# Kernel tuning notes

Hardware: AMD Instinct MI355X
Metric: run time of the kernel (lower is better)

## Reference

```python
import jax, jax.numpy as jnp
import numpy as np

L = 8        # number of node layers in the DAG
D = 64       # width of every node layer
B = 262144   # batch
N_CONN = L * (L - 1) // 2  # 28 all-to-all forward connections


def setup_inputs() -> dict:
    key = jax.random.key(0)
    kx, kw, kb = jax.random.split(key, 3)
    x = jax.random.normal(kx, (B, D), dtype=jnp.float32)
    # connection weights, torch Linear convention: y = x @ W.T + b, W is [out, in]
    Ws = jax.random.normal(kw, (N_CONN, D, D), dtype=jnp.float32) * (1.0 / np.sqrt(D))
    bs = jax.random.normal(kb, (N_CONN, D), dtype=jnp.float32) * 0.1
    return {"x": x, "Ws": Ws, "bs": bs}


def reference(x, Ws, bs):
    # outputs[0] = input; outputs[1..L-1] start at zero and accumulate messages.
    outs = [x] + [jnp.zeros((x.shape[0], D), dtype=x.dtype) for _ in range(L - 1)]
    # Same iteration order as the torch double loop: source i ascending,
    # target offset i2 ascending; connection c maps layer i -> layer i+i2+1.
    c = 0
    for i in range(L):
        for i2 in range(L - 1 - i):
            j = i + i2 + 1
            outs[j] = outs[j] + jax.nn.relu(outs[i] @ Ws[c].T + bs[c])
            c += 1
    return outs[L - 1]
```

## Files before the change

### kernel.cpp

```cpp
#include <hip/hip_runtime.h>


#define DD 64
#define NCONN 28
#define THREADS 256
#define ROWS_PER_WAVE 32
#define ROWS_PER_BLOCK 128
#define MAT_ELEMS 4096

typedef __bf16 bf16x8 __attribute__((ext_vector_type(8)));
typedef float f32x4 __attribute__((ext_vector_type(4)));
typedef unsigned short u16x8 __attribute__((ext_vector_type(8)));

__device__ constexpr int OFFS[7] = {0, 7, 13, 18, 22, 25, 27};
__device__ constexpr int CONN[28] = {0, 1,7, 2,8,13, 3,9,14,18, 4,10,15,19,22,
                                     5,11,16,20,23,25, 6,12,17,21,24,26,27};

__device__ __forceinline__ unsigned short f2bfu(float f) {
    return __builtin_bit_cast(unsigned short, (__bf16)f);
}

__device__ __forceinline__ f32x4 vmax4(f32x4 a, f32x4 b) {
#if __has_builtin(__builtin_elementwise_max)
    return __builtin_elementwise_max(a, b);
#else
    f32x4 r;
    r[0] = fmaxf(a[0], b[0]); r[1] = fmaxf(a[1], b[1]);
    r[2] = fmaxf(a[2], b[2]); r[3] = fmaxf(a[3], b[3]);
    return r;
#endif
}

__device__ __forceinline__ void gll16(const unsigned short* g, unsigned short* l) {
    __builtin_amdgcn_global_load_lds(
        (const __attribute__((address_space(1))) unsigned int*)g,
        (__attribute__((address_space(3))) unsigned int*)l, 16, 0, 0);
}

__global__ void wconv_kernel(const float* __restrict__ w,
                             unsigned short* __restrict__ o) {
    int i = blockIdx.x * blockDim.x + threadIdx.x;
    if (i >= NCONN * 512) return;
    int conn = i >> 9;
    int within = i & 511;
    int r  = within >> 3;
    int k0 = (within & 7) << 3;
    const float* src = w + conn * MAT_ELEMS + r * DD + k0;
    float4 v0 = *reinterpret_cast<const float4*>(src);
    float4 v1 = *reinterpret_cast<const float4*>(src + 4);
    u16x8 d;
    d[0] = f2bfu(v0.x); d[1] = f2bfu(v0.y); d[2] = f2bfu(v0.z); d[3] = f2bfu(v0.w);
    d[4] = f2bfu(v1.x); d[5] = f2bfu(v1.y); d[6] = f2bfu(v1.z); d[7] = f2bfu(v1.w);
    *reinterpret_cast<u16x8*>(o + conn * MAT_ELEMS + r * DD + (k0 ^ ((r & 7) << 3))) = d;
}

template <bool GLL>
__global__ __launch_bounds__(THREADS, 2)
void dag_kernel(const float* __restrict__ x,
                const float* __restrict__ Wf,
                const unsigned short* __restrict__ Wimg,
                const float* __restrict__ bs,
                float* __restrict__ out) {
    __shared__ __align__(16) unsigned short ring[4 * MAT_ELEMS];
    __shared__ __align__(16) unsigned short sB[4 * 1024];
    __shared__ __align__(16) float sBias[NCONN * DD];

    const int tid  = threadIdx.x;
    const int lane = tid & 63;
    const int wv   = tid >> 6;
    const int l15  = lane & 15;
    const int kg   = lane >> 4;

    const long rowbase = (long)blockIdx.x * ROWS_PER_BLOCK + wv * ROWS_PER_WAVE;

    for (int idx = tid; idx < NCONN * DD / 4; idx += THREADS)
        reinterpret_cast<float4*>(sBias)[idx] = reinterpret_cast<const float4*>(bs)[idx];

    bf16x8 afrag[7][2][2];
#pragma unroll
    for (int rt = 0; rt < 2; ++rt) {
        const float* xr = x + (rowbase + rt * 16 + l15) * DD;
#pragma unroll
        for (int s = 0; s < 2; ++s) {
            float4 v0 = *reinterpret_cast<const float4*>(xr + s * 32 + kg * 8);
            float4 v1 = *reinterpret_cast<const float4*>(xr + s * 32 + kg * 8 + 4);
            bf16x8 f;
            f[0] = (__bf16)v0.x; f[1] = (__bf16)v0.y; f[2] = (__bf16)v0.z; f[3] = (__bf16)v0.w;
            f[4] = (__bf16)v1.x; f[5] = (__bf16)v1.y; f[6] = (__bf16)v1.z; f[7] = (__bf16)v1.w;
            afrag[0][rt][s] = f;
        }
    }

    auto stage_gll = [&](int p) {
        const unsigned short* src = Wimg + CONN[p] * MAT_ELEMS + wv * 512 + lane * 8;
        unsigned short* dst = ring + (p & 3) * MAT_ELEMS + wv * 512;
#pragma unroll
        for (int h = 0; h < 2; ++h)
            gll16(src + h * 2048, dst + h * 2048);
    };
    auto stage_direct = [&](int p) {
        const float* wp = Wf + CONN[p] * MAT_ELEMS;
#pragma unroll
        for (int h = 0; h < 2; ++h) {
            const int e0 = h * 2048 + tid * 8;
            float4 a0 = *reinterpret_cast<const float4*>(wp + e0);
            float4 a1 = *reinterpret_cast<const float4*>(wp + e0 + 4);
            u16x8 d;
            d[0] = f2bfu(a0.x); d[1] = f2bfu(a0.y); d[2] = f2bfu(a0.z); d[3] = f2bfu(a0.w);
            d[4] = f2bfu(a1.x); d[5] = f2bfu(a1.y); d[6] = f2bfu(a1.z); d[7] = f2bfu(a1.w);
            const int r = e0 >> 6, k0 = e0 & 63;
            *reinterpret_cast<u16x8*>(ring + (p & 3) * MAT_ELEMS +
                                      r * DD + (k0 ^ ((r & 7) << 3))) = d;
        }
    };

    if constexpr (GLL) { stage_gll(0); stage_gll(1); }
    __syncthreads();

    unsigned short* myB = sB + wv * 1024;
    f32x4 acc[2][4];

#pragma unroll
    for (int j = 1; j <= 7; ++j) {
#pragma unroll
        for (int rt = 0; rt < 2; ++rt)
#pragma unroll
            for (int t = 0; t < 4; ++t) {
                acc[rt][t][0] = 0.f; acc[rt][t][1] = 0.f;
                acc[rt][t][2] = 0.f; acc[rt][t][3] = 0.f;
            }

#pragma unroll
        for (int i = 0; i < j; ++i) {
            const int p = j * (j - 1) / 2 + i;
            const int c = OFFS[i] + (j - i - 1);

            if constexpr (GLL) {
                if ((p & 1) == 0) {
                    if (p > 0) __syncthreads();
                    if (p + 2 < NCONN) stage_gll(p + 2);
                    if (p + 3 < NCONN) stage_gll(p + 3);
                }
            } else {
                __syncthreads();
                stage_direct(p);
                __syncthreads();
            }

            const unsigned short* wsl = ring + (p & 3) * MAT_ELEMS;
            __builtin_amdgcn_s_setprio(1);
#pragma unroll
            for (int t = 0; t < 4; ++t) {
                const int n  = t * 16 + l15;
                const int xo = (n & 7) << 3;
                u16x8 rw0 = *reinterpret_cast<const u16x8*>(wsl + n * DD + ((kg * 8) ^ xo));
                u16x8 rw1 = *reinterpret_cast<const u16x8*>(wsl + n * DD + ((32 + kg * 8) ^ xo));
                const float bv = sBias[c * DD + n];
                const f32x4 bv4 = {bv, bv, bv, bv};
#pragma unroll
                for (int rt = 0; rt < 2; ++rt) {
                    f32x4 C = acc[rt][t] + bv4;
                    C = __builtin_amdgcn_mfma_f32_16x16x32_bf16(
                            afrag[i][rt][0], __builtin_bit_cast(bf16x8, rw0), C, 0, 0, 0);
                    C = __builtin_amdgcn_mfma_f32_16x16x32_bf16(
                            afrag[i][rt][1], __builtin_bit_cast(bf16x8, rw1), C, 0, 0, 0);
                    acc[rt][t] = vmax4(C, acc[rt][t]);
                }
            }
            __builtin_amdgcn_s_setprio(0);
        }

        if (j < 7) {
#pragma unroll
            for (int rt = 0; rt < 2; ++rt) {
#pragma unroll
                for (int t = 0; t < 4; ++t) {
                    const int n = t * 16 + l15;
#pragma unroll
                    for (int q = 0; q < 4; ++q) {
                        const int mr = kg * 4 + q;
                        myB[mr * DD + (n ^ ((mr & 7) << 3))] = f2bfu(acc[rt][t][q]);
                    }
                }
                asm volatile("s_waitcnt lgkmcnt(0)" ::: "memory");
#pragma unroll
                for (int s = 0; s < 2; ++s) {
                    u16x8 ra = *reinterpret_cast<const u16x8*>(
                        &myB[l15 * DD + ((s * 32 + kg * 8) ^ ((l15 & 7) << 3))]);
                    afrag[j][rt][s] = __builtin_bit_cast(bf16x8, ra);
                }
                asm volatile("s_waitcnt lgkmcnt(0)" ::: "memory");
            }
        } else {
            float* orow = out + rowbase * DD;
#pragma unroll
            for (int rt = 0; rt < 2; ++rt)
#pragma unroll
                for (int t = 0; t < 4; ++t)
#pragma unroll
                    for (int q = 0; q < 4; ++q)
                        orow[(rt * 16 + kg * 4 + q) * DD + t * 16 + l15] = acc[rt][t][q];
        }
    }
}

extern "C" void kernel_launch(void* const* d_in, const int* in_sizes, int n_in,
                              void* d_out, int out_size, void* d_ws, size_t ws_size,
                              hipStream_t stream) {
    const float* x  = (const float*)d_in[0];
    const float* Ws = (const float*)d_in[1];
    const float* bs = (const float*)d_in[2];
    float* out = (float*)d_out;

    const int nrows = in_sizes[0] / DD;
    const int grid  = nrows / ROWS_PER_BLOCK;

    const size_t wbf_bytes = (size_t)NCONN * MAT_ELEMS * sizeof(unsigned short);
    if (ws_size >= wbf_bytes) {
        unsigned short* wbf = (unsigned short*)d_ws;
        wconv_kernel<<<(NCONN * 512 + 255) / 256, 256, 0, stream>>>(Ws, wbf);
        dag_kernel<true><<<grid, THREADS, 0, stream>>>(x, Ws, wbf, bs, out);
    } else {
        dag_kernel<false><<<grid, THREADS, 0, stream>>>(x, Ws, nullptr, bs, out);
    }
}
```

Before: 103.7 us.

## Load weights directly into registers with double buffering instead of LDS ring

Removes the LDS weight ring and the global_load_lds staging, and with them the block-wide barriers. Each wave now loads its B-operand fragments for the next connection straight from global (L2-resident) memory into a register double buffer, and reads biases directly from global. The weight image is stored unswizzled, the bias add moves after the MFMAs, and the explicit lgkmcnt waits around the per-wave LDS transpose are dropped. The aim is to cut LDS traffic and synchronisation, at the cost of more VGPRs (two 8-vector buffers) and more global load traffic per wave, which may hurt occupancy.

```diff
diff --git a/kernel.cpp b/kernel.cpp
--- a/kernel.cpp
+++ b/kernel.cpp
@@ -31,39 +31,27 @@
 #endif
 }
 
-__device__ __forceinline__ void gll16(const unsigned short* g, unsigned short* l) {
-    __builtin_amdgcn_global_load_lds(
-        (const __attribute__((address_space(1))) unsigned int*)g,
-        (__attribute__((address_space(3))) unsigned int*)l, 16, 0, 0);
-}
-
 __global__ void wconv_kernel(const float* __restrict__ w,
                              unsigned short* __restrict__ o) {
     int i = blockIdx.x * blockDim.x + threadIdx.x;
     if (i >= NCONN * 512) return;
-    int conn = i >> 9;
-    int within = i & 511;
-    int r  = within >> 3;
-    int k0 = (within & 7) << 3;
-    const float* src = w + conn * MAT_ELEMS + r * DD + k0;
+    const float* src = w + i * 8;
     float4 v0 = *reinterpret_cast<const float4*>(src);
     float4 v1 = *reinterpret_cast<const float4*>(src + 4);
     u16x8 d;
     d[0] = f2bfu(v0.x); d[1] = f2bfu(v0.y); d[2] = f2bfu(v0.z); d[3] = f2bfu(v0.w);
     d[4] = f2bfu(v1.x); d[5] = f2bfu(v1.y); d[6] = f2bfu(v1.z); d[7] = f2bfu(v1.w);
-    *reinterpret_cast<u16x8*>(o + conn * MAT_ELEMS + r * DD + (k0 ^ ((r & 7) << 3))) = d;
-}
-
-template <bool GLL>
+    *reinterpret_cast<u16x8*>(o + i * 8) = d;
+}
+
+template <bool BF16IMG>
 __global__ __launch_bounds__(THREADS, 2)
 void dag_kernel(const float* __restrict__ x,
                 const float* __restrict__ Wf,
                 const unsigned short* __restrict__ Wimg,
                 const float* __restrict__ bs,
                 float* __restrict__ out) {
-    __shared__ __align__(16) unsigned short ring[4 * MAT_ELEMS];
     __shared__ __align__(16) unsigned short sB[4 * 1024];
-    __shared__ __align__(16) float sBias[NCONN * DD];
 
     const int tid  = threadIdx.x;
     const int lane = tid & 63;
@@ -72,9 +60,6 @@
     const int kg   = lane >> 4;
 
     const long rowbase = (long)blockIdx.x * ROWS_PER_BLOCK + wv * ROWS_PER_WAVE;
-
-    for (int idx = tid; idx < NCONN * DD / 4; idx += THREADS)
-        reinterpret_cast<float4*>(sBias)[idx] = reinterpret_cast<const float4*>(bs)[idx];
 
     bf16x8 afrag[7][2][2];
 #pragma unroll
@@ -91,31 +76,34 @@
         }
     }
 
-    auto stage_gll = [&](int p) {
-        const unsigned short* src = Wimg + CONN[p] * MAT_ELEMS + wv * 512 + lane * 8;
-        unsigned short* dst = ring + (p & 3) * MAT_ELEMS + wv * 512;
-#pragma unroll
-        for (int h = 0; h < 2; ++h)
-            gll16(src + h * 2048, dst + h * 2048);
+    u16x8 wbufA[8], wbufB[8];
+
+    auto loadW = [&](int p, u16x8* dst) {
+        if constexpr (BF16IMG) {
+            const unsigned short* base = Wimg + CONN[p] * MAT_ELEMS + l15 * DD + kg * 8;
+#pragma unroll
+            for (int t = 0; t < 4; ++t)
+#pragma unroll
+                for (int s = 0; s < 2; ++s)
+                    dst[t * 2 + s] = *reinterpret_cast<const u16x8*>(
+                        base + t * 16 * DD + s * 32);
+        } else {
+            const float* base = Wf + CONN[p] * MAT_ELEMS + l15 * DD + kg * 8;
+#pragma unroll
+            for (int t = 0; t < 4; ++t)
+#pragma unroll
+                for (int s = 0; s < 2; ++s) {
+                    float4 v0 = *reinterpret_cast<const float4*>(base + t * 16 * DD + s * 32);
+                    float4 v1 = *reinterpret_cast<const float4*>(base + t * 16 * DD + s * 32 + 4);
+                    u16x8 d;
+                    d[0] = f2bfu(v0.x); d[1] = f2bfu(v0.y); d[2] = f2bfu(v0.z); d[3] = f2bfu(v0.w);
+                    d[4] = f2bfu(v1.x); d[5] = f2bfu(v1.y); d[6] = f2bfu(v1.z); d[7] = f2bfu(v1.w);
+                    dst[t * 2 + s] = d;
+                }
+        }
     };
-    auto stage_direct = [&](int p) {
-        const float* wp = Wf + CONN[p] * MAT_ELEMS;
-#pragma unroll
-        for (int h = 0; h < 2; ++h) {
-            const int e0 = h * 2048 + tid * 8;
-            float4 a0 = *reinterpret_cast<const float4*>(wp + e0);
-            float4 a1 = *reinterpret_cast<const float4*>(wp + e0 + 4);
-            u16x8 d;
-            d[0] = f2bfu(a0.x); d[1] = f2bfu(a0.y); d[2] = f2bfu(a0.z); d[3] = f2bfu(a0.w);
-            d[4] = f2bfu(a1.x); d[5] = f2bfu(a1.y); d[6] = f2bfu(a1.z); d[7] = f2bfu(a1.w);
-            const int r = e0 >> 6, k0 = e0 & 63;
-            *reinterpret_cast<u16x8*>(ring + (p & 3) * MAT_ELEMS +
-                                      r * DD + (k0 ^ ((r & 7) << 3))) = d;
-        }
-    };
-
-    if constexpr (GLL) { stage_gll(0); stage_gll(1); }
-    __syncthreads();
+
+    loadW(0, wbufA);
 
     unsigned short* myB = sB + wv * 1024;
     f32x4 acc[2][4];
@@ -134,37 +122,27 @@
         for (int i = 0; i < j; ++i) {
             const int p = j * (j - 1) / 2 + i;
             const int c = OFFS[i] + (j - i - 1);
-
-            if constexpr (GLL) {
-                if ((p & 1) == 0) {
-                    if (p > 0) __syncthreads();
-                    if (p + 2 < NCONN) stage_gll(p + 2);
-                    if (p + 3 < NCONN) stage_gll(p + 3);
-                }
-            } else {
-                __syncthreads();
-                stage_direct(p);
-                __syncthreads();
-            }
-
-            const unsigned short* wsl = ring + (p & 3) * MAT_ELEMS;
+            u16x8* wcur = (p & 1) ? wbufB : wbufA;
+            u16x8* wnxt = (p & 1) ? wbufA : wbufB;
+
+            if (p + 1 < NCONN) loadW(p + 1, wnxt);
+
+            const float* bp = bs + c * DD + l15;
+            float bv0 = bp[0], bv1 = bp[16], bv2 = bp[32], bv3 = bp[48];
+            float bvv[4] = {bv0, bv1, bv2, bv3};
+
             __builtin_amdgcn_s_setprio(1);
 #pragma unroll
             for (int t = 0; t < 4; ++t) {
-                const int n  = t * 16 + l15;
-                const int xo = (n & 7) << 3;
-                u16x8 rw0 = *reinterpret_cast<const u16x8*>(wsl + n * DD + ((kg * 8) ^ xo));
-                u16x8 rw1 = *reinterpret_cast<const u16x8*>(wsl + n * DD + ((32 + kg * 8) ^ xo));
-                const float bv = sBias[c * DD + n];
-                const f32x4 bv4 = {bv, bv, bv, bv};
+                const f32x4 b4 = {bvv[t], bvv[t], bvv[t], bvv[t]};
 #pragma unroll
                 for (int rt = 0; rt < 2; ++rt) {
-                    f32x4 C = acc[rt][t] + bv4;
+                    f32x4 C = acc[rt][t];
                     C = __builtin_amdgcn_mfma_f32_16x16x32_bf16(
-                            afrag[i][rt][0], __builtin_bit_cast(bf16x8, rw0), C, 0, 0, 0);
+                            afrag[i][rt][0], __builtin_bit_cast(bf16x8, wcur[t * 2 + 0]), C, 0, 0, 0);
                     C = __builtin_amdgcn_mfma_f32_16x16x32_bf16(
-                            afrag[i][rt][1], __builtin_bit_cast(bf16x8, rw1), C, 0, 0, 0);
-                    acc[rt][t] = vmax4(C, acc[rt][t]);
+                            afrag[i][rt][1], __builtin_bit_cast(bf16x8, wcur[t * 2 + 1]), C, 0, 0, 0);
+                    acc[rt][t] = vmax4(C + b4, acc[rt][t]);
                 }
             }
             __builtin_amdgcn_s_setprio(0);
@@ -182,14 +160,12 @@
                         myB[mr * DD + (n ^ ((mr & 7) << 3))] = f2bfu(acc[rt][t][q]);
                     }
                 }
-                asm volatile("s_waitcnt lgkmcnt(0)" ::: "memory");
 #pragma unroll
                 for (int s = 0; s < 2; ++s) {
                     u16x8 ra = *reinterpret_cast<const u16x8*>(
                         &myB[l15 * DD + ((s * 32 + kg * 8) ^ ((l15 & 7) << 3))]);
                     afrag[j][rt][s] = __builtin_bit_cast(bf16x8, ra);
                 }
-                asm volatile("s_waitcnt lgkmcnt(0)" ::: "memory");
             }
         } else {
             float* orow = out + rowbase * DD;
```

New measurement: 226.7 us. 119% more time.

## Halve block size, prefetch bias into registers, drop LDS bias table and waitcnts

Applied to the files above, without the earlier changes.

Shrinks the block to two waves handling 64 rows, so each wave stages twice as much of every weight matrix, and removes the shared bias table. Bias values for upcoming connections are now loaded from global memory into a double-buffered register array alongside the weight prefetch, and the bias is added after the MFMAs rather than before. The explicit LDS waitcnt fences around the per-wave restaging of activations are removed. The aim is lower LDS use for higher occupancy and fewer LDS reads in the inner loop, at the cost of more blocks, more global bias loads per block, and reliance on the compiler to order the wave-private LDS write/read correctly.

```diff
diff --git a/kernel.cpp b/kernel.cpp
--- a/kernel.cpp
+++ b/kernel.cpp
@@ -3,9 +3,9 @@
 
 #define DD 64
 #define NCONN 28
-#define THREADS 256
+#define THREADS 128
 #define ROWS_PER_WAVE 32
-#define ROWS_PER_BLOCK 128
+#define ROWS_PER_BLOCK 64
 #define MAT_ELEMS 4096
 
 typedef __bf16 bf16x8 __attribute__((ext_vector_type(8)));
@@ -62,8 +62,7 @@
                 const float* __restrict__ bs,
                 float* __restrict__ out) {
     __shared__ __align__(16) unsigned short ring[4 * MAT_ELEMS];
-    __shared__ __align__(16) unsigned short sB[4 * 1024];
-    __shared__ __align__(16) float sBias[NCONN * DD];
+    __shared__ __align__(16) unsigned short sB[2 * 1024];
 
     const int tid  = threadIdx.x;
     const int lane = tid & 63;
@@ -72,9 +71,6 @@
     const int kg   = lane >> 4;
 
     const long rowbase = (long)blockIdx.x * ROWS_PER_BLOCK + wv * ROWS_PER_WAVE;
-
-    for (int idx = tid; idx < NCONN * DD / 4; idx += THREADS)
-        reinterpret_cast<float4*>(sBias)[idx] = reinterpret_cast<const float4*>(bs)[idx];
 
     bf16x8 afrag[7][2][2];
 #pragma unroll
@@ -91,18 +87,27 @@
         }
     }
 
+    float breg[2][2][4];
+    auto loadBias = [&](int p) {
+        const float* bp = bs + CONN[p] * DD + l15;
+        float* b = breg[(p >> 1) & 1][p & 1];
+        b[0] = bp[0]; b[1] = bp[16]; b[2] = bp[32]; b[3] = bp[48];
+    };
+
     auto stage_gll = [&](int p) {
-        const unsigned short* src = Wimg + CONN[p] * MAT_ELEMS + wv * 512 + lane * 8;
-        unsigned short* dst = ring + (p & 3) * MAT_ELEMS + wv * 512;
-#pragma unroll
-        for (int h = 0; h < 2; ++h)
-            gll16(src + h * 2048, dst + h * 2048);
+        const unsigned short* src = Wimg + CONN[p] * MAT_ELEMS + lane * 8;
+        unsigned short* dst = ring + (p & 3) * MAT_ELEMS + lane * 8;
+#pragma unroll
+        for (int h = 0; h < 4; ++h) {
+            const int off = (wv * 4 + h) * 512;
+            gll16(src + off, dst + off);
+        }
     };
     auto stage_direct = [&](int p) {
         const float* wp = Wf + CONN[p] * MAT_ELEMS;
 #pragma unroll
-        for (int h = 0; h < 2; ++h) {
-            const int e0 = h * 2048 + tid * 8;
+        for (int h = 0; h < 4; ++h) {
+            const int e0 = h * 1024 + tid * 8;
             float4 a0 = *reinterpret_cast<const float4*>(wp + e0);
             float4 a1 = *reinterpret_cast<const float4*>(wp + e0 + 4);
             u16x8 d;
@@ -114,6 +119,7 @@
         }
     };
 
+    loadBias(0); loadBias(1);
     if constexpr (GLL) { stage_gll(0); stage_gll(1); }
     __syncthreads();
 
@@ -133,21 +139,22 @@
 #pragma unroll
         for (int i = 0; i < j; ++i) {
             const int p = j * (j - 1) / 2 + i;
-            const int c = OFFS[i] + (j - i - 1);
 
             if constexpr (GLL) {
                 if ((p & 1) == 0) {
                     if (p > 0) __syncthreads();
-                    if (p + 2 < NCONN) stage_gll(p + 2);
-                    if (p + 3 < NCONN) stage_gll(p + 3);
+                    if (p + 2 < NCONN) { loadBias(p + 2); loadBias(p + 3); }
+                    if (p + 2 < NCONN) { stage_gll(p + 2); stage_gll(p + 3); }
                 }
             } else {
                 __syncthreads();
                 stage_direct(p);
+                loadBias(p);
                 __syncthreads();
             }
 
             const unsigned short* wsl = ring + (p & 3) * MAT_ELEMS;
+            const float* bv = breg[(p >> 1) & 1][p & 1];
             __builtin_amdgcn_s_setprio(1);
 #pragma unroll
             for (int t = 0; t < 4; ++t) {
@@ -155,16 +162,15 @@
                 const int xo = (n & 7) << 3;
                 u16x8 rw0 = *reinterpret_cast<const u16x8*>(wsl + n * DD + ((kg * 8) ^ xo));
                 u16x8 rw1 = *reinterpret_cast<const u16x8*>(wsl + n * DD + ((32 + kg * 8) ^ xo));
-                const float bv = sBias[c * DD + n];
-                const f32x4 bv4 = {bv, bv, bv, bv};
+                const f32x4 b4 = {bv[t], bv[t], bv[t], bv[t]};
 #pragma unroll
                 for (int rt = 0; rt < 2; ++rt) {
-                    f32x4 C = acc[rt][t] + bv4;
+                    f32x4 C = acc[rt][t];
                     C = __builtin_amdgcn_mfma_f32_16x16x32_bf16(
                             afrag[i][rt][0], __builtin_bit_cast(bf16x8, rw0), C, 0, 0, 0);
                     C = __builtin_amdgcn_mfma_f32_16x16x32_bf16(
                             afrag[i][rt][1], __builtin_bit_cast(bf16x8, rw1), C, 0, 0, 0);
-                    acc[rt][t] = vmax4(C, acc[rt][t]);
+                    acc[rt][t] = vmax4(C + b4, acc[rt][t]);
                 }
             }
             __builtin_amdgcn_s_setprio(0);
@@ -182,14 +188,12 @@
                         myB[mr * DD + (n ^ ((mr & 7) << 3))] = f2bfu(acc[rt][t][q]);
                     }
                 }
-                asm volatile("s_waitcnt lgkmcnt(0)" ::: "memory");
 #pragma unroll
                 for (int s = 0; s < 2; ++s) {
                     u16x8 ra = *reinterpret_cast<const u16x8*>(
                         &myB[l15 * DD + ((s * 32 + kg * 8) ^ ((l15 & 7) << 3))]);
                     afrag[j][rt][s] = __builtin_bit_cast(bf16x8, ra);
                 }
-                asm volatile("s_waitcnt lgkmcnt(0)" ::: "memory");
             }
         } else {
             float* orow = out + rowbase * DD;
```

Result: slower. 109.0 us (+5.0%).

## Split output columns across wave pairs to halve per-wave accumulators and raise occupancy

Applied to the files above, without the earlier changes.

Each block now handles 64 rows, with pairs of waves sharing 32 rows and each wave computing half of the 64 output columns. This halves the accumulator registers per wave and raises the launch bound to 3 blocks per SM for more occupancy. The price is twice as many blocks, each reloading all 28 weight matrices into LDS, plus block-wide barriers after every layer to exchange activations through shared memory. The bias add also moves to after the MFMAs.

```diff
diff --git a/kernel.cpp b/kernel.cpp
--- a/kernel.cpp
+++ b/kernel.cpp
@@ -4,8 +4,7 @@
 #define DD 64
 #define NCONN 28
 #define THREADS 256
-#define ROWS_PER_WAVE 32
-#define ROWS_PER_BLOCK 128
+#define ROWS_PER_BLOCK 64
 #define MAT_ELEMS 4096
 
 typedef __bf16 bf16x8 __attribute__((ext_vector_type(8)));
@@ -35,6 +34,12 @@
     __builtin_amdgcn_global_load_lds(
         (const __attribute__((address_space(1))) unsigned int*)g,
         (__attribute__((address_space(3))) unsigned int*)l, 16, 0, 0);
+}
+
+__device__ __forceinline__ void lds_barrier() {
+    asm volatile("s_waitcnt lgkmcnt(0)" ::: "memory");
+    __builtin_amdgcn_s_barrier();
+    asm volatile("" ::: "memory");
 }
 
 __global__ void wconv_kernel(const float* __restrict__ w,
@@ -55,23 +60,25 @@
 }
 
 template <bool GLL>
-__global__ __launch_bounds__(THREADS, 2)
+__global__ __launch_bounds__(THREADS, 3)
 void dag_kernel(const float* __restrict__ x,
                 const float* __restrict__ Wf,
                 const unsigned short* __restrict__ Wimg,
                 const float* __restrict__ bs,
                 float* __restrict__ out) {
     __shared__ __align__(16) unsigned short ring[4 * MAT_ELEMS];
-    __shared__ __align__(16) unsigned short sB[4 * 1024];
+    __shared__ __align__(16) unsigned short sB[2 * 2048];
     __shared__ __align__(16) float sBias[NCONN * DD];
 
     const int tid  = threadIdx.x;
     const int lane = tid & 63;
     const int wv   = tid >> 6;
+    const int pair = wv >> 1;
+    const int h    = wv & 1;
     const int l15  = lane & 15;
     const int kg   = lane >> 4;
 
-    const long rowbase = (long)blockIdx.x * ROWS_PER_BLOCK + wv * ROWS_PER_WAVE;
+    const long rowbase = (long)blockIdx.x * ROWS_PER_BLOCK + pair * 32;
 
     for (int idx = tid; idx < NCONN * DD / 4; idx += THREADS)
         reinterpret_cast<float4*>(sBias)[idx] = reinterpret_cast<const float4*>(bs)[idx];
@@ -95,14 +102,14 @@
         const unsigned short* src = Wimg + CONN[p] * MAT_ELEMS + wv * 512 + lane * 8;
         unsigned short* dst = ring + (p & 3) * MAT_ELEMS + wv * 512;
 #pragma unroll
-        for (int h = 0; h < 2; ++h)
-            gll16(src + h * 2048, dst + h * 2048);
+        for (int hh = 0; hh < 2; ++hh)
+            gll16(src + hh * 2048, dst + hh * 2048);
     };
     auto stage_direct = [&](int p) {
         const float* wp = Wf + CONN[p] * MAT_ELEMS;
 #pragma unroll
-        for (int h = 0; h < 2; ++h) {
-            const int e0 = h * 2048 + tid * 8;
+        for (int hh = 0; hh < 2; ++hh) {
+            const int e0 = hh * 2048 + tid * 8;
             float4 a0 = *reinterpret_cast<const float4*>(wp + e0);
             float4 a1 = *reinterpret_cast<const float4*>(wp + e0 + 4);
             u16x8 d;
@@ -117,15 +124,15 @@
     if constexpr (GLL) { stage_gll(0); stage_gll(1); }
     __syncthreads();
 
-    unsigned short* myB = sB + wv * 1024;
-    f32x4 acc[2][4];
+    unsigned short* myPB = sB + pair * 2048;
+    f32x4 acc[2][2];
 
 #pragma unroll
     for (int j = 1; j <= 7; ++j) {
 #pragma unroll
         for (int rt = 0; rt < 2; ++rt)
 #pragma unroll
-            for (int t = 0; t < 4; ++t) {
+            for (int t = 0; t < 2; ++t) {
                 acc[rt][t][0] = 0.f; acc[rt][t][1] = 0.f;
                 acc[rt][t][2] = 0.f; acc[rt][t][3] = 0.f;
             }
@@ -138,8 +145,7 @@
             if constexpr (GLL) {
                 if ((p & 1) == 0) {
                     if (p > 0) __syncthreads();
-                    if (p + 2 < NCONN) stage_gll(p + 2);
-                    if (p + 3 < NCONN) stage_gll(p + 3);
+                    if (p + 2 < NCONN) { stage_gll(p + 2); stage_gll(p + 3); }
                 }
             } else {
                 __syncthreads();
@@ -150,21 +156,21 @@
             const unsigned short* wsl = ring + (p & 3) * MAT_ELEMS;
             __builtin_amdgcn_s_setprio(1);
 #pragma unroll
-            for (int t = 0; t < 4; ++t) {
-                const int n  = t * 16 + l15;
+            for (int t = 0; t < 2; ++t) {
+                const int n  = h * 32 + t * 16 + l15;
                 const int xo = (n & 7) << 3;
                 u16x8 rw0 = *reinterpret_cast<const u16x8*>(wsl + n * DD + ((kg * 8) ^ xo));
                 u16x8 rw1 = *reinterpret_cast<const u16x8*>(wsl + n * DD + ((32 + kg * 8) ^ xo));
                 const float bv = sBias[c * DD + n];
-                const f32x4 bv4 = {bv, bv, bv, bv};
+                const f32x4 b4 = {bv, bv, bv, bv};
 #pragma unroll
                 for (int rt = 0; rt < 2; ++rt) {
-                    f32x4 C = acc[rt][t] + bv4;
+                    f32x4 C = acc[rt][t];
                     C = __builtin_amdgcn_mfma_f32_16x16x32_bf16(
                             afrag[i][rt][0], __builtin_bit_cast(bf16x8, rw0), C, 0, 0, 0);
                     C = __builtin_amdgcn_mfma_f32_16x16x32_bf16(
                             afrag[i][rt][1], __builtin_bit_cast(bf16x8, rw1), C, 0, 0, 0);
-                    acc[rt][t] = vmax4(C, acc[rt][t]);
+                    acc[rt][t] = vmax4(C + b4, acc[rt][t]);
                 }
             }
             __builtin_amdgcn_s_setprio(0);
@@ -172,34 +178,36 @@
 
         if (j < 7) {
 #pragma unroll
-            for (int rt = 0; rt < 2; ++rt) {
-#pragma unroll
-                for (int t = 0; t < 4; ++t) {
-                    const int n = t * 16 + l15;
+            for (int rt = 0; rt < 2; ++rt)
+#pragma unroll
+                for (int t = 0; t < 2; ++t) {
+                    const int f = h * 32 + t * 16 + l15;
 #pragma unroll
                     for (int q = 0; q < 4; ++q) {
-                        const int mr = kg * 4 + q;
-                        myB[mr * DD + (n ^ ((mr & 7) << 3))] = f2bfu(acc[rt][t][q]);
+                        const int mr = rt * 16 + kg * 4 + q;
+                        myPB[mr * DD + (f ^ ((mr & 7) << 3))] = f2bfu(acc[rt][t][q]);
                     }
                 }
-                asm volatile("s_waitcnt lgkmcnt(0)" ::: "memory");
+            lds_barrier();
+#pragma unroll
+            for (int rt = 0; rt < 2; ++rt)
 #pragma unroll
                 for (int s = 0; s < 2; ++s) {
                     u16x8 ra = *reinterpret_cast<const u16x8*>(
-                        &myB[l15 * DD + ((s * 32 + kg * 8) ^ ((l15 & 7) << 3))]);
+                        &myPB[(rt * 16 + l15) * DD + ((s * 32 + kg * 8) ^ ((l15 & 7) << 3))]);
                     afrag[j][rt][s] = __builtin_bit_cast(bf16x8, ra);
                 }
-                asm volatile("s_waitcnt lgkmcnt(0)" ::: "memory");
-            }
+            lds_barrier();
         } else {
             float* orow = out + rowbase * DD;
 #pragma unroll
             for (int rt = 0; rt < 2; ++rt)
 #pragma unroll
-                for (int t = 0; t < 4; ++t)
+                for (int t = 0; t < 2; ++t)
 #pragma unroll
                     for (int q = 0; q < 4; ++q)
-                        orow[(rt * 16 + kg * 4 + q) * DD + t * 16 + l15] = acc[rt][t][q];
+                        orow[(rt * 16 + kg * 4 + q) * DD + h * 32 + t * 16 + l15] =
+                            acc[rt][t][q];
         }
     }
 }
```

Result: no change. 102.4 us (-1.3%).
